# Kernel optimization log

Hardware: AMD Instinct MI355X
Metric: run time of the kernel (lower is better)

Reference implementation:

```python
import jax, jax.numpy as jnp
import numpy as np

N_HEAD = 8
TANH_CLIP = 10.0
NEG = jnp.float32(-1e9)


def setup_inputs() -> dict:
    key = jax.random.key(0)
    ks = jax.random.split(key, 10)
    B, N, E = 128, 1000, 128
    s = lambda k, shape: (jax.random.normal(k, shape, dtype=jnp.float32) * 0.05)
    return dict(
        node_embeddings=s(ks[0], (B, N, E)),
        graph_embedding=s(ks[1], (B, E)),
        Wqkv=s(ks[2], (E, 3 * E)), bqkv=s(ks[3], (3 * E,)),
        Wfix=s(ks[4], (E, E)), bfix=s(ks[5], (E,)),
        Wstep=s(ks[6], (2 * E, E)), bstep=s(ks[7], (E,)),
        Wmlp=s(ks[8], (E, E)), bmlp=s(ks[9], (E,)),
    )


def reference(node_embeddings, graph_embedding, Wqkv, bqkv, Wfix, bfix,
              Wstep, bstep, Wmlp, bmlp):
    B, N, E = node_embeddings.shape
    H = N_HEAD
    d = E // H
    scale = 1.0 / jnp.sqrt(jnp.float32(d))

    # shared projections (done once, like the torch code)
    qkv = node_embeddings @ Wqkv + bqkv               # [B,N,3E]
    k, v, logit_k = jnp.split(qkv, 3, axis=-1)        # each [B,N,E]
    kh = k.reshape(B, N, H, d).transpose(0, 2, 1, 3)  # [B,H,N,d]
    vh = v.reshape(B, N, H, d).transpose(0, 2, 1, 3)  # [B,H,N,d]
    fixed = graph_embedding @ Wfix + bfix             # [B,E]
    first = node_embeddings[:, 0, :]                  # [B,E]

    init_cur = jnp.zeros((B,), jnp.int32)             # depot = node 0
    init_mask = jnp.zeros((B, N), bool).at[:, 0].set(True)  # True = visited/masked
    batch_idx = jnp.arange(B)

    def step(carry, _):
        cur, mask, total = carry
        last = jnp.take_along_axis(node_embeddings, cur[:, None, None], axis=1)[:, 0, :]  # [B,E]
        q = fixed + jnp.concatenate([first, last], axis=-1) @ Wstep + bstep               # [B,E]
        qh = q.reshape(B, H, d)
        attn = jnp.einsum('bhd,bhnd->bhn', qh, kh) * scale
        attn = jnp.where(mask[:, None, :], NEG, attn)
        attn = jax.nn.softmax(attn, axis=-1)
        ctx = jnp.einsum('bhn,bhnd->bhd', attn, vh).reshape(B, E)
        x = ctx @ Wmlp + bmlp
        logits = jnp.einsum('be,bne->bn', x, logit_k) * scale
        logits = jnp.tanh(logits) * TANH_CLIP
        logits = jnp.where(mask, NEG, logits)
        log_p = jax.nn.log_softmax(logits, axis=-1)
        act = jnp.argmax(log_p, axis=-1).astype(jnp.int32)   # greedy decode
        lp = jnp.take_along_axis(log_p, act[:, None], axis=-1)[:, 0]
        new_mask = mask.at[batch_idx, act].set(True)
        return (act, new_mask, total + lp), act

    (cur, mask, total), seq = jax.lax.scan(
        step, (init_cur, init_mask, jnp.zeros((B,), jnp.float32)), None, length=N - 1)
    # total: summed log-prob of selected tour, [B] (matches _log_p_ in torch code)
    return total
```

## Files before the change

### kernel.cpp

```cpp
#include <hip/hip_runtime.h>
#include <hip/hip_fp16.h>

constexpr int kB = 128;
constexpr int kN = 1000;
constexpr int kE = 128;
constexpr int kH = 8;
constexpr float kFP8Scale = 64.f;
constexpr float kQKScale = 0.25f / 64.f;

typedef _Float16 h2 __attribute__((ext_vector_type(2)));
typedef float f2 __attribute__((ext_vector_type(2)));

__device__ __forceinline__ float fast_tanh(float x) {
  float t = __expf(2.f * x);
  return 1.f - 2.f / (t + 1.f);
}

__device__ __forceinline__ unsigned char enc_fp8(float v) {
  unsigned p = __builtin_amdgcn_cvt_pk_fp8_f32(v, v, 0, false);
  return (unsigned char)(p & 0xFF);
}

__device__ __forceinline__ void dotp(unsigned u, f2 qa, f2 qb, f2& sacc) {
  f2 lo = __builtin_amdgcn_cvt_pk_f32_fp8(u, false);
  f2 hi = __builtin_amdgcn_cvt_pk_f32_fp8(u, true);
  sacc += lo * qa;
  sacc += hi * qb;
}
__device__ __forceinline__ float dot16p(uint4 tq, const f2* q2) {
  f2 s = {0.f, 0.f};
  dotp(tq.x, q2[0], q2[1], s);
  dotp(tq.y, q2[2], q2[3], s);
  dotp(tq.z, q2[4], q2[5], s);
  dotp(tq.w, q2[6], q2[7], s);
  return s.x + s.y;
}
__device__ __forceinline__ void vaccp(unsigned u, f2 hv2, f2& a0, f2& a1) {
  f2 lo = __builtin_amdgcn_cvt_pk_f32_fp8(u, false);
  f2 hi = __builtin_amdgcn_cvt_pk_f32_fp8(u, true);
  a0 += hv2 * lo;
  a1 += hv2 * hi;
}
__device__ __forceinline__ void unpack16(uint4 a, uint4 b, f2* q2) {
  unsigned w[8] = {a.x, a.y, a.z, a.w, b.x, b.y, b.z, b.w};
#pragma unroll
  for (int i = 0; i < 8; ++i) {
    h2 hh = __builtin_bit_cast(h2, w[i]);
    q2[i] = f2{(float)hh.x, (float)hh.y};
  }
}

__device__ __forceinline__ void maxcomb(float& m, int& a, float mo, int ao) {
  bool take = (mo > m) || (mo == m && ao < a);
  m = take ? mo : m;
  a = take ? ao : a;
}

template <int CTRL>
__device__ __forceinline__ float dpp_bcastf(float x) {
  return __builtin_bit_cast(
      float, __builtin_amdgcn_update_dpp(0, __builtin_bit_cast(int, x), CTRL,
                                         0xf, 0xf, true));
}
template <int CTRL>
__device__ __forceinline__ int dpp_bcasti(int x) {
  return __builtin_amdgcn_update_dpp(0, x, CTRL, 0xf, 0xf, true);
}
template <int CTRL>
__device__ __forceinline__ float dpp_addf(float x) {
  return x + dpp_bcastf<CTRL>(x);
}
template <int CTRL>
__device__ __forceinline__ void dpp_maxcomb(float& m, int& a) {
  float mo = dpp_bcastf<CTRL>(m);
  int ao = dpp_bcasti<CTRL>(a);
  maxcomb(m, a, mo, ao);
}

__device__ __forceinline__ void barrier_lds() {
  asm volatile("s_waitcnt lgkmcnt(0)" ::: "memory");
  __builtin_amdgcn_s_barrier();
  asm volatile("" ::: "memory");
}

__global__ __launch_bounds__(384) void qkv_kernel(
    const float* __restrict__ ne, const float* __restrict__ Wqkv,
    const float* __restrict__ bqkv, unsigned char* __restrict__ kq,
    unsigned char* __restrict__ vq, unsigned char* __restrict__ lkq) {
  __shared__ float rows[16 * kE];
  int b = blockIdx.x;
  int n0 = blockIdx.y * 16;
  int ntile = min(16, kN - n0);
  int tid = threadIdx.x;

  for (int idx = tid; idx < ntile * kE; idx += 384)
    rows[idx] = ne[(b * kN + n0) * kE + idx];
  __syncthreads();

  int j = tid;
  float acc[16];
#pragma unroll
  for (int r = 0; r < 16; ++r) acc[r] = 0.f;
  for (int i = 0; i < kE; ++i) {
    float w = Wqkv[i * (3 * kE) + j];
#pragma unroll
    for (int r = 0; r < 16; ++r) acc[r] += rows[r * kE + i] * w;
  }
  float bias = bqkv[j];
  unsigned char* dst;
  int col;
  if (j < kE) { dst = kq; col = j; }
  else if (j < 2 * kE) { dst = vq; col = j - kE; }
  else { dst = lkq; col = j - 2 * kE; }
  for (int r = 0; r < ntile; ++r)
    dst[(size_t)(b * kN + n0 + r) * kE + col] =
        enc_fp8((acc[r] + bias) * kFP8Scale);
}

__global__ __launch_bounds__(128) void qbase_kernel(
    const float* __restrict__ ne, const float* __restrict__ ge,
    const float* __restrict__ Wfix, const float* __restrict__ bfix,
    const float* __restrict__ Wstep, const float* __restrict__ bstep,
    float* __restrict__ qbase) {
  __shared__ float g[kE], f[kE];
  int b = blockIdx.x, e = threadIdx.x;
  g[e] = ge[b * kE + e];
  f[e] = ne[(size_t)b * kN * kE + e];
  __syncthreads();
  float acc = bfix[e] + bstep[e];
  for (int i = 0; i < kE; ++i)
    acc += g[i] * Wfix[i * kE + e] + f[i] * Wstep[i * kE + e];
  qbase[b * kE + e] = acc;
}

__global__ __launch_bounds__(128) void qstep_kernel(
    const float* __restrict__ ne, const float* __restrict__ Wstep,
    const float* __restrict__ qbase, __half* __restrict__ qstep) {
  __shared__ float rows[8 * kE];
  int b = blockIdx.x;
  int n0 = blockIdx.y * 8;
  int tid = threadIdx.x;
  const float* Wbot = Wstep + kE * kE;

  for (int idx = tid; idx < 8 * kE; idx += 128)
    rows[idx] = ne[((size_t)b * kN + n0) * kE + idx];
  __syncthreads();

  float acc[8];
#pragma unroll
  for (int r = 0; r < 8; ++r) acc[r] = 0.f;
  for (int i = 0; i < kE; ++i) {
    float w = Wbot[i * kE + tid];
#pragma unroll
    for (int r = 0; r < 8; ++r) acc[r] += rows[r * kE + i] * w;
  }
  float qb = qbase[b * kE + tid];
#pragma unroll
  for (int r = 0; r < 8; ++r)
    qstep[((size_t)b * kN + n0 + r) * kE + tid] =
        __float2half((qb + acc[r]) * kQKScale);
}

__global__ __launch_bounds__(1024) void rollout_kernel(
    const float* __restrict__ Wmlp, const float* __restrict__ bmlp,
    const unsigned char* __restrict__ kq, const unsigned char* __restrict__ vq,
    const unsigned char* __restrict__ lkq, const __half* __restrict__ qstep,
    float* __restrict__ out) {
  __shared__ __align__(16) int rem[1024];
  __shared__ __align__(16) float parts[kE][65];
  __shared__ __align__(16) float wmT[kE][140];
  __shared__ float bm[kE];
  __shared__ __align__(16) float ctx[kE];
  __shared__ __align__(16) __half xh[kE];
  __shared__ float redSum[16][kH];
  __shared__ __align__(16) float4 redPack[16];

  int b = blockIdx.x;
  int tid = threadIdx.x;
  int lane = tid & 63;
  int wave = tid >> 6;
  int g = tid >> 3;
  int t = tid & 7;

  const unsigned char* kqb = kq + (size_t)b * kN * kE;
  const unsigned char* vqb = vq + (size_t)b * kN * kE;
  const unsigned char* lqb = lkq + (size_t)b * kN * kE;
  const __half* qsb = qstep + (size_t)b * kN * kE;

#pragma unroll
  for (int m = 0; m < 16; ++m) {
    int idx = tid * 16 + m;
    wmT[idx & 127][idx >> 7] = Wmlp[idx];
  }
  rem[tid] = (tid < kN - 1) ? tid + 1 : kN - 1;
  if (tid < kE) bm[tid] = bmlp[tid];

  int A = 0;
  uint4 qa, qb_;
  {
    const uint4* qr = (const uint4*)qsb;
    qa = qr[2 * t];
    qb_ = qr[2 * t + 1];
  }
  float total = 0.f;

  int jn[8];
#pragma unroll
  for (int r = 0; r < 8; ++r) {
    int j = g + 128 * r;
    jn[r] = (j < kN - 1) ? j + 1 : -1;
  }

  barrier_lds();

  for (int step = 0; step < kN - 1; ++step) {
    int R = kN - 1 - step;

    uint4 kb0, vb0, kb1, vb1;
    if (jn[0] >= 0) {
      kb0 = ((const uint4*)(kqb + (size_t)jn[0] * kE))[t];
      vb0 = ((const uint4*)(vqb + (size_t)jn[0] * kE))[t];
    }
    if (jn[1] >= 0) {
      kb1 = ((const uint4*)(kqb + (size_t)jn[1] * kE))[t];
      vb1 = ((const uint4*)(vqb + (size_t)jn[1] * kE))[t];
    }
    f2 q2[8];
    unpack16(qa, qb_, q2);
    f2 acc2[8];
#pragma unroll
    for (int i = 0; i < 8; ++i) acc2[i] = f2{0.f, 0.f};
    float den = 0.f;
#pragma unroll
    for (int r = 0; r < 8; ++r) {
      if (jn[r] < 0) break;
      uint4 kk = (r & 1) ? kb1 : kb0;
      uint4 vv = (r & 1) ? vb1 : vb0;
      if (r + 2 < 8 && jn[r + 2] >= 0) {
        if (r & 1) {
          kb1 = ((const uint4*)(kqb + (size_t)jn[r + 2] * kE))[t];
          vb1 = ((const uint4*)(vqb + (size_t)jn[r + 2] * kE))[t];
        } else {
          kb0 = ((const uint4*)(kqb + (size_t)jn[r + 2] * kE))[t];
          vb0 = ((const uint4*)(vqb + (size_t)jn[r + 2] * kE))[t];
        }
      }
      float s = dot16p(kk, q2);
      float hv = __expf(s);
      den += hv;
      f2 hv2 = {hv, hv};
      vaccp(vv.x, hv2, acc2[0], acc2[1]);
      vaccp(vv.y, hv2, acc2[2], acc2[3]);
      vaccp(vv.z, hv2, acc2[4], acc2[5]);
      vaccp(vv.w, hv2, acc2[6], acc2[7]);
    }
    uint4 lu[8];
#pragma unroll
    for (int r = 0; r < 8; ++r)
      if (jn[r] >= 0) lu[r] = ((const uint4*)(lqb + (size_t)jn[r] * kE))[t];
    den = dpp_addf<0x128>(den);
    den += __shfl_xor(den, 16);
    den += __shfl_xor(den, 32);
    if (lane < kH) redSum[wave][lane] = den;
    {
      float av[16];
#pragma unroll
      for (int c = 0; c < 4; ++c) {
        av[4 * c + 0] = acc2[2 * c].x;
        av[4 * c + 1] = acc2[2 * c].y;
        av[4 * c + 2] = acc2[2 * c + 1].x;
        av[4 * c + 3] = acc2[2 * c + 1].y;
      }
#pragma unroll
      for (int i = 0; i < 16; ++i) av[i] = dpp_addf<0x128>(av[i]);
      if (((lane >> 3) & 1) == 0) {
        int chunk = wave * 4 + (lane >> 4);
#pragma unroll
        for (int i = 0; i < 16; ++i)
          parts[t * 16 + i][(chunk + 4 * t) & 63] = av[i];
      }
    }
    barrier_lds();

    {
      int e = tid >> 3, k = tid & 7, hh = e >> 4;
      float s = 0.f;
#pragma unroll
      for (int m = 0; m < 8; ++m)
        s += parts[e][((8 * k + m) + 4 * hh) & 63];
      float d = redSum[2 * k][hh] + redSum[2 * k + 1][hh];
      s = dpp_addf<0xB1>(s);
      s = dpp_addf<0x4E>(s);
      s = dpp_addf<0x141>(s);
      d = dpp_addf<0xB1>(d);
      d = dpp_addf<0x4E>(d);
      d = dpp_addf<0x141>(d);
      if (k == 0) ctx[e] = s / (d * kFP8Scale);
    }
    barrier_lds();

    {
      float xacc = 0.f;
      const float4* c4 = (const float4*)(ctx + t * 16);
      const float4* w4 = (const float4*)(&wmT[g][t * 16]);
#pragma unroll
      for (int k4 = 0; k4 < 4; ++k4) {
        float4 cv = c4[k4];
        float4 wv = w4[k4];
        xacc += cv.x * wv.x + cv.y * wv.y + cv.z * wv.z + cv.w * wv.w;
      }
      xacc = dpp_addf<0xB1>(xacc);
      xacc = dpp_addf<0x4E>(xacc);
      xacc = dpp_addf<0x141>(xacc);
      if (t == 0) xh[g] = __float2half((bm[g] + xacc) * kQKScale);
    }
    barrier_lds();

    int myv = rem[tid];
    int nxt = rem[(tid < 1023) ? tid + 1 : 1023];
    int pra[8], prb[8];
#pragma unroll
    for (int r = 0; r < 8; ++r) {
      int j = g + 128 * r;
      pra[r] = rem[j];
      prb[r] = rem[(j < 1023) ? j + 1 : 1023];
    }
    float m0 = -1e30f;
    int arg = 0x7fffffff;
    {
      f2 x2[8];
      uint4 xv0 = ((const uint4*)xh)[2 * t];
      uint4 xv1 = ((const uint4*)xh)[2 * t + 1];
      unpack16(xv0, xv1, x2);
#pragma unroll
      for (int r = 0; r < 8; ++r)
        if (jn[r] >= 0) {
          float s = dot16p(lu[r], x2);
          s = dpp_addf<0xB1>(s);
          s = dpp_addf<0x4E>(s);
          s = dpp_addf<0x141>(s);
          if (t == r) {
            m0 = fast_tanh(s) * 10.f;
            arg = jn[r];
          }
        }
    }
    float M = m0;
    int argM = arg;
    dpp_maxcomb<0xB1>(M, argM);
    dpp_maxcomb<0x4E>(M, argM);
    dpp_maxcomb<0x141>(M, argM);
    dpp_maxcomb<0x128>(M, argM);
#pragma unroll
    for (int off = 16; off <= 32; off <<= 1) {
      float mo = __shfl_xor(M, off);
      int ao = __shfl_xor(argM, off);
      maxcomb(M, argM, mo, ao);
    }
    float ex = __expf(m0 - M);
    ex = dpp_addf<0xB1>(ex);
    ex = dpp_addf<0x4E>(ex);
    ex = dpp_addf<0x141>(ex);
    ex = dpp_addf<0x128>(ex);
    ex += __shfl_xor(ex, 16);
    ex += __shfl_xor(ex, 32);
    if (lane == 0)
      redPack[wave] = make_float4(M, ex, __int_as_float(argM), 0.f);
    barrier_lds();

    {
      float4 rp = redPack[lane & 15];
      float mw = rp.x, sw = rp.y;
      int aw = __float_as_int(rp.z);
      float Mf = mw;
      int Af = aw;
      dpp_maxcomb<0xB1>(Mf, Af);
      dpp_maxcomb<0x4E>(Mf, Af);
      dpp_maxcomb<0x141>(Mf, Af);
      dpp_maxcomb<0x128>(Mf, Af);
      A = Af;
      const uint4* qr = (const uint4*)(qsb + (size_t)A * kE);
      qa = qr[2 * t];
      qb_ = qr[2 * t + 1];
      float sc = sw * __expf(mw - Mf);
      sc = dpp_addf<0xB1>(sc);
      sc = dpp_addf<0x4E>(sc);
      sc = dpp_addf<0x141>(sc);
      sc = dpp_addf<0x128>(sc);
      total += -logf(sc);
      int Rn = R - 1;
#pragma unroll
      for (int r = 0; r < 8; ++r) {
        int j = g + 128 * r;
        jn[r] = (j < Rn) ? ((pra[r] < A) ? pra[r] : prb[r]) : -1;
      }
      if (tid < R - 1 && myv >= A) rem[tid] = nxt;
    }
  }
  if (tid == 0) out[b] = total;
}

extern "C" void kernel_launch(void* const* d_in, const int* in_sizes, int n_in,
                              void* d_out, int out_size, void* d_ws,
                              size_t ws_size, hipStream_t stream) {
  const float* ne = (const float*)d_in[0];
  const float* ge = (const float*)d_in[1];
  const float* Wqkv = (const float*)d_in[2];
  const float* bqkv = (const float*)d_in[3];
  const float* Wfix = (const float*)d_in[4];
  const float* bfix = (const float*)d_in[5];
  const float* Wstep = (const float*)d_in[6];
  const float* bstep = (const float*)d_in[7];
  const float* Wmlp = (const float*)d_in[8];
  const float* bmlp = (const float*)d_in[9];
  float* out = (float*)d_out;

  size_t nkv = (size_t)kB * kN * kE;
  unsigned char* kq = (unsigned char*)d_ws;
  unsigned char* vq = kq + nkv;
  unsigned char* lkq = vq + nkv;
  __half* qstep = (__half*)(lkq + nkv);
  float* qbase = (float*)(qstep + nkv);

  qkv_kernel<<<dim3(kB, (kN + 15) / 16), 384, 0, stream>>>(ne, Wqkv, bqkv, kq,
                                                           vq, lkq);
  qbase_kernel<<<kB, kE, 0, stream>>>(ne, ge, Wfix, bfix, Wstep, bstep, qbase);
  qstep_kernel<<<dim3(kB, kN / 8), 128, 0, stream>>>(ne, Wstep, qbase, qstep);
  rollout_kernel<<<kB, 1024, 0, stream>>>(Wmlp, bmlp, kq, vq, lkq, qstep, out);
}
```

Measured before the change: 8.676 ms.

## Fold Wmlp into logit keys to remove per-step MLP matvec

Uses associativity to precompute logit_k·Wmlpᵀ per node (an fp8 m2 tensor) plus a per-node bias term. The rollout step then dots ctx directly against these folded keys, which removes the in-loop ctx@Wmlp matvec and one barrier per decode step. The logit projection drops out of the qkv kernel. Two extra precompute kernels and extra workspace are added, and fp8 quantisation now applies to the folded product, which may shift numerics.

```diff
diff --git a/kernel.cpp b/kernel.cpp
--- a/kernel.cpp
+++ b/kernel.cpp
@@ -83,17 +83,17 @@
   asm volatile("" ::: "memory");
 }
 
-__global__ __launch_bounds__(384) void qkv_kernel(
+__global__ __launch_bounds__(256) void qkv_kernel(
     const float* __restrict__ ne, const float* __restrict__ Wqkv,
     const float* __restrict__ bqkv, unsigned char* __restrict__ kq,
-    unsigned char* __restrict__ vq, unsigned char* __restrict__ lkq) {
+    unsigned char* __restrict__ vq) {
   __shared__ float rows[16 * kE];
   int b = blockIdx.x;
   int n0 = blockIdx.y * 16;
   int ntile = min(16, kN - n0);
   int tid = threadIdx.x;
 
-  for (int idx = tid; idx < ntile * kE; idx += 384)
+  for (int idx = tid; idx < ntile * kE; idx += 256)
     rows[idx] = ne[(b * kN + n0) * kE + idx];
   __syncthreads();
 
@@ -110,11 +110,78 @@
   unsigned char* dst;
   int col;
   if (j < kE) { dst = kq; col = j; }
-  else if (j < 2 * kE) { dst = vq; col = j - kE; }
-  else { dst = lkq; col = j - 2 * kE; }
+  else { dst = vq; col = j - kE; }
   for (int r = 0; r < ntile; ++r)
     dst[(size_t)(b * kN + n0 + r) * kE + col] =
         enc_fp8((acc[r] + bias) * kFP8Scale);
+}
+
+__global__ __launch_bounds__(128) void w3_kernel(
+    const float* __restrict__ Wqkv, const float* __restrict__ bqkv,
+    const float* __restrict__ Wmlp, const float* __restrict__ bmlp,
+    float* __restrict__ W3, float* __restrict__ b3, float* __restrict__ w4,
+    float* __restrict__ c4) {
+  __shared__ float lk_s[kE];
+  __shared__ float red[kE];
+  int gin = blockIdx.x, i = threadIdx.x;
+  lk_s[i] = Wqkv[gin * (3 * kE) + 2 * kE + i];
+  __syncthreads();
+  float s = 0.f;
+  for (int g = 0; g < kE; ++g) s += lk_s[g] * Wmlp[i * kE + g];
+  W3[gin * kE + i] = s;
+  red[i] = lk_s[i] * bmlp[i];
+  __syncthreads();
+  if (i == 0) {
+    float t = 0.f;
+    for (int g = 0; g < kE; ++g) t += red[g];
+    w4[gin] = t;
+  }
+  if (gin == 0) {
+    float t2 = 0.f;
+    for (int g = 0; g < kE; ++g) t2 += bqkv[2 * kE + g] * Wmlp[i * kE + g];
+    b3[i] = t2;
+    if (i == 0) {
+      float t3 = 0.f;
+      for (int g = 0; g < kE; ++g) t3 += bqkv[2 * kE + g] * bmlp[g];
+      c4[0] = t3;
+    }
+  }
+}
+
+__global__ __launch_bounds__(128) void m2_kernel(
+    const float* __restrict__ ne, const float* __restrict__ W3,
+    const float* __restrict__ b3, const float* __restrict__ w4,
+    const float* __restrict__ c4, unsigned char* __restrict__ m2q,
+    float* __restrict__ bB) {
+  __shared__ float rows[8 * kE];
+  __shared__ float w4_s[kE];
+  int b = blockIdx.x;
+  int n0 = blockIdx.y * 8;
+  int tid = threadIdx.x;
+
+  for (int idx = tid; idx < 8 * kE; idx += 128)
+    rows[idx] = ne[((size_t)b * kN + n0) * kE + idx];
+  w4_s[tid] = w4[tid];
+  __syncthreads();
+
+  float acc[8];
+#pragma unroll
+  for (int r = 0; r < 8; ++r) acc[r] = 0.f;
+  for (int gin = 0; gin < kE; ++gin) {
+    float w = W3[gin * kE + tid];
+#pragma unroll
+    for (int r = 0; r < 8; ++r) acc[r] += rows[r * kE + gin] * w;
+  }
+  float bi = b3[tid];
+#pragma unroll
+  for (int r = 0; r < 8; ++r)
+    m2q[(size_t)(b * kN + n0 + r) * kE + tid] =
+        enc_fp8((acc[r] + bi) * kFP8Scale);
+  if (tid < 8) {
+    float s = c4[0];
+    for (int g = 0; g < kE; ++g) s += rows[tid * kE + g] * w4_s[g];
+    bB[b * kN + n0 + tid] = 0.25f * s;
+  }
 }
 
 __global__ __launch_bounds__(128) void qbase_kernel(
@@ -162,16 +229,13 @@
 }
 
 __global__ __launch_bounds__(1024) void rollout_kernel(
-    const float* __restrict__ Wmlp, const float* __restrict__ bmlp,
     const unsigned char* __restrict__ kq, const unsigned char* __restrict__ vq,
-    const unsigned char* __restrict__ lkq, const __half* __restrict__ qstep,
-    float* __restrict__ out) {
+    const unsigned char* __restrict__ m2q, const __half* __restrict__ qstep,
+    const float* __restrict__ bB, float* __restrict__ out) {
   __shared__ __align__(16) int rem[1024];
   __shared__ __align__(16) float parts[kE][65];
-  __shared__ __align__(16) float wmT[kE][140];
-  __shared__ float bm[kE];
+  __shared__ __align__(16) float bb_s[1024];
   __shared__ __align__(16) float ctx[kE];
-  __shared__ __align__(16) __half xh[kE];
   __shared__ float redSum[16][kH];
   __shared__ __align__(16) float4 redPack[16];
 
@@ -184,16 +248,11 @@
 
   const unsigned char* kqb = kq + (size_t)b * kN * kE;
   const unsigned char* vqb = vq + (size_t)b * kN * kE;
-  const unsigned char* lqb = lkq + (size_t)b * kN * kE;
+  const unsigned char* mqb = m2q + (size_t)b * kN * kE;
   const __half* qsb = qstep + (size_t)b * kN * kE;
 
-#pragma unroll
-  for (int m = 0; m < 16; ++m) {
-    int idx = tid * 16 + m;
-    wmT[idx & 127][idx >> 7] = Wmlp[idx];
-  }
+  if (tid < kN) bb_s[tid] = bB[(size_t)b * kN + tid];
   rem[tid] = (tid < kN - 1) ? tid + 1 : kN - 1;
-  if (tid < kE) bm[tid] = bmlp[tid];
 
   int A = 0;
   uint4 qa, qb_;
@@ -254,10 +313,10 @@
       vaccp(vv.z, hv2, acc2[4], acc2[5]);
       vaccp(vv.w, hv2, acc2[6], acc2[7]);
     }
-    uint4 lu[8];
+    uint4 mu[8];
 #pragma unroll
     for (int r = 0; r < 8; ++r)
-      if (jn[r] >= 0) lu[r] = ((const uint4*)(lqb + (size_t)jn[r] * kE))[t];
+      if (jn[r] >= 0) mu[r] = ((const uint4*)(mqb + (size_t)jn[r] * kE))[t];
     den = dpp_addf<0x128>(den);
     den += __shfl_xor(den, 16);
     den += __shfl_xor(den, 32);
@@ -299,23 +358,6 @@
     }
     barrier_lds();
 
-    {
-      float xacc = 0.f;
-      const float4* c4 = (const float4*)(ctx + t * 16);
-      const float4* w4 = (const float4*)(&wmT[g][t * 16]);
-#pragma unroll
-      for (int k4 = 0; k4 < 4; ++k4) {
-        float4 cv = c4[k4];
-        float4 wv = w4[k4];
-        xacc += cv.x * wv.x + cv.y * wv.y + cv.z * wv.z + cv.w * wv.w;
-      }
-      xacc = dpp_addf<0xB1>(xacc);
-      xacc = dpp_addf<0x4E>(xacc);
-      xacc = dpp_addf<0x141>(xacc);
-      if (t == 0) xh[g] = __float2half((bm[g] + xacc) * kQKScale);
-    }
-    barrier_lds();
-
     int myv = rem[tid];
     int nxt = rem[(tid < 1023) ? tid + 1 : 1023];
     int pra[8], prb[8];
@@ -325,26 +367,33 @@
       pra[r] = rem[j];
       prb[r] = rem[(j < 1023) ? j + 1 : 1023];
     }
-    float m0 = -1e30f;
+    float m0raw = 0.f;
     int arg = 0x7fffffff;
     {
-      f2 x2[8];
-      uint4 xv0 = ((const uint4*)xh)[2 * t];
-      uint4 xv1 = ((const uint4*)xh)[2 * t + 1];
-      unpack16(xv0, xv1, x2);
+      f2 c2[8];
+      const float4* cc = (const float4*)(ctx + t * 16);
+#pragma unroll
+      for (int k4 = 0; k4 < 4; ++k4) {
+        float4 cv = cc[k4];
+        c2[2 * k4] = f2{cv.x, cv.y};
+        c2[2 * k4 + 1] = f2{cv.z, cv.w};
+      }
 #pragma unroll
       for (int r = 0; r < 8; ++r)
         if (jn[r] >= 0) {
-          float s = dot16p(lu[r], x2);
+          float s = dot16p(mu[r], c2);
           s = dpp_addf<0xB1>(s);
           s = dpp_addf<0x4E>(s);
           s = dpp_addf<0x141>(s);
           if (t == r) {
-            m0 = fast_tanh(s) * 10.f;
+            m0raw = s;
             arg = jn[r];
           }
         }
     }
+    float m0 = -1e30f;
+    if (arg != 0x7fffffff)
+      m0 = fast_tanh(kQKScale * m0raw + bb_s[arg]) * 10.f;
     float M = m0;
     int argM = arg;
     dpp_maxcomb<0xB1>(M, argM);
@@ -418,13 +467,20 @@
   size_t nkv = (size_t)kB * kN * kE;
   unsigned char* kq = (unsigned char*)d_ws;
   unsigned char* vq = kq + nkv;
-  unsigned char* lkq = vq + nkv;
-  __half* qstep = (__half*)(lkq + nkv);
+  unsigned char* m2q = vq + nkv;
+  __half* qstep = (__half*)(m2q + nkv);
   float* qbase = (float*)(qstep + nkv);
-
-  qkv_kernel<<<dim3(kB, (kN + 15) / 16), 384, 0, stream>>>(ne, Wqkv, bqkv, kq,
-                                                           vq, lkq);
+  float* bB = qbase + kB * kE;
+  float* W3 = bB + (size_t)kB * kN;
+  float* b3 = W3 + kE * kE;
+  float* w4 = b3 + kE;
+  float* c4 = w4 + kE;
+
+  qkv_kernel<<<dim3(kB, (kN + 15) / 16), 256, 0, stream>>>(ne, Wqkv, bqkv, kq,
+                                                           vq);
+  w3_kernel<<<kE, kE, 0, stream>>>(Wqkv, bqkv, Wmlp, bmlp, W3, b3, w4, c4);
   qbase_kernel<<<kB, kE, 0, stream>>>(ne, ge, Wfix, bfix, Wstep, bstep, qbase);
   qstep_kernel<<<dim3(kB, kN / 8), 128, 0, stream>>>(ne, Wstep, qbase, qstep);
-  rollout_kernel<<<kB, 1024, 0, stream>>>(Wmlp, bmlp, kq, vq, lkq, qstep, out);
-}
+  m2_kernel<<<dim3(kB, kN / 8), 128, 0, stream>>>(ne, W3, b3, w4, c4, m2q, bB);
+  rollout_kernel<<<kB, 1024, 0, stream>>>(kq, vq, m2q, qstep, bB, out);
+}
```

New measurement: 7.299 ms. -15.9%, faster.
